# Kernel optimization log

Measured on AMD Instinct MI355X. Metric: run time of the kernel, lower is better.

Reference implementation:

```python
import jax, jax.numpy as jnp
import numpy as np

IP = 10  # power-iteration steps


def setup_inputs() -> dict:
    key = jax.random.key(0)
    k1, k2 = jax.random.split(key)
    B, C, H, W = 16, 512, 64, 64
    x = jax.random.normal(k1, (B, C, H, W), dtype=jnp.float32)
    # random start vector for power iteration (torch: FloatTensor.normal_(0,1))
    v = jax.random.normal(k2, (B, C, 1), dtype=jnp.float32)
    return {"x": x, "v": v}


def reference(x, v):
    B, C, H, W = x.shape
    # w = x.view(B,C,HW).permute(0,2,1) -> (B, HW, C)
    w = jnp.transpose(x.reshape(B, C, H * W), (0, 2, 1))
    # W_s = w^T w : (B, C, C)
    Ws = jnp.einsum('bnc,bnd->bcd', w, w)

    def step(vc, _):
        vc = jnp.matmul(Ws, vc)                                   # (B,C,1)
        vc = vc / jnp.linalg.norm(vc, axis=(1, 2), keepdims=True)  # per-batch L2 norm
        return vc, None

    v, _ = jax.lax.scan(step, v, None, length=IP)
    # u = W v, normalized : (B, HW, 1)
    u = jnp.matmul(w, v)
    u = u / jnp.linalg.norm(u, axis=(1, 2), keepdims=True)
    # z = u v^T : (B, HW, C) -> (B, C, H, W)
    z = jnp.matmul(u, jnp.transpose(v, (0, 2, 1)))
    z = jnp.transpose(z, (0, 2, 1)).reshape(B, C, H, W)
    return x + z
```

## Files before the change

kernel.cpp:

```cpp
#include <hip/hip_runtime.h>
#include <stdint.h>

#define NB 16
#define NC 512
#define NHW 4096

typedef unsigned short u16;
typedef __bf16 bf16x8 __attribute__((ext_vector_type(8)));
typedef float f32x4 __attribute__((ext_vector_type(4)));
typedef unsigned short u16x8 __attribute__((ext_vector_type(8)));
typedef unsigned short u16x4 __attribute__((ext_vector_type(4)));

#define AS1 __attribute__((address_space(1)))
#define AS3 __attribute__((address_space(3)))

__device__ __forceinline__ float bf2f(u16 h) {
    union { unsigned u; float f; } a; a.u = ((unsigned)h) << 16; return a.f;
}
__device__ __forceinline__ u16 f2bf(float f) {
    union { float f; unsigned u; } a; a.f = f;
    unsigned u = a.u;
    return (u16)((u + 0x7FFFu + ((u >> 16) & 1u)) >> 16);
}

__global__ __launch_bounds__(256) void k_to_bf16(const float* __restrict__ x,
                                                 u16* __restrict__ xb) {
    int i = blockIdx.x * 256 + threadIdx.x;
    f32x4 v = ((const f32x4*)x)[i];
    u16x4 o;
    o[0] = f2bf(v[0]); o[1] = f2bf(v[1]); o[2] = f2bf(v[2]); o[3] = f2bf(v[3]);
    ((u16x4*)xb)[i] = o;
}

__global__ __launch_bounds__(256, 1)
void k_gemm_bt(const u16* __restrict__ Ab, const u16* __restrict__ Bb,
               u16* __restrict__ Cb, int K, int N,
               size_t sA, size_t sB, size_t sC, float scale) {
    __shared__ u16 As[4][128 * 32];
    __shared__ u16 Bs[4][128 * 32];
    const int tid = threadIdx.x;
    const int wave = tid >> 6, lane = tid & 63;
    const int b = blockIdx.z;
    const u16* A  = Ab + (size_t)b * sA + (size_t)blockIdx.x * 128 * K;
    const u16* Bm = Bb + (size_t)b * sB + (size_t)blockIdx.y * 128 * K;

    const int srow = tid >> 2;
    const int scol = ((tid & 3) ^ ((srow >> 1) & 3)) * 8;
    const u16* ag0 = A  + (size_t)srow * K + scol;
    const u16* ag1 = ag0 + (size_t)64 * K;
    const u16* bg0 = Bm + (size_t)srow * K + scol;
    const u16* bg1 = bg0 + (size_t)64 * K;

#define STAGE(BUF, KO)                                                         \
    {                                                                          \
        __builtin_amdgcn_global_load_lds((AS1 void*)(ag0 + (KO)),              \
            (AS3 void*)(&As[BUF][wave * 512]), 16, 0, 0);                      \
        __builtin_amdgcn_global_load_lds((AS1 void*)(ag1 + (KO)),              \
            (AS3 void*)(&As[BUF][2048 + wave * 512]), 16, 0, 0);               \
        __builtin_amdgcn_global_load_lds((AS1 void*)(bg0 + (KO)),              \
            (AS3 void*)(&Bs[BUF][wave * 512]), 16, 0, 0);                      \
        __builtin_amdgcn_global_load_lds((AS1 void*)(bg1 + (KO)),              \
            (AS3 void*)(&Bs[BUF][2048 + wave * 512]), 16, 0, 0);               \
    }

    f32x4 acc[4][4];
#pragma unroll
    for (int i = 0; i < 4; i++)
#pragma unroll
        for (int j = 0; j < 4; j++) acc[i][j] = f32x4{0.f, 0.f, 0.f, 0.f};

    const int rm = (wave & 1) * 64;
    const int rn = (wave >> 1) * 64;
    const int m16 = lane & 15, quad = lane >> 4;
    const int qsw8 = (quad ^ ((m16 >> 1) & 3)) * 8;

#define COMPUTE(BUF)                                                           \
    {                                                                          \
        bf16x8 af[4], bfr[4];                                                  \
        _Pragma("unroll")                                                      \
        for (int mi = 0; mi < 4; mi++)                                         \
            af[mi] = *(const bf16x8*)&As[BUF][(rm + mi * 16 + m16) * 32 +      \
                                             qsw8];                            \
        _Pragma("unroll")                                                      \
        for (int ni = 0; ni < 4; ni++)                                         \
            bfr[ni] = *(const bf16x8*)&Bs[BUF][(rn + ni * 16 + m16) * 32 +     \
                                              qsw8];                           \
        _Pragma("unroll")                                                      \
        for (int mi = 0; mi < 4; mi++)                                         \
            _Pragma("unroll")                                                  \
            for (int ni = 0; ni < 4; ni++)                                     \
                acc[mi][ni] = __builtin_amdgcn_mfma_f32_16x16x32_bf16(         \
                    af[mi], bfr[ni], acc[mi][ni], 0, 0, 0);                    \
    }

#define PHASE(J, KNEXT)                                                        \
    asm volatile("s_waitcnt vmcnt(12)" ::: "memory");                          \
    __builtin_amdgcn_s_barrier();                                              \
    __builtin_amdgcn_sched_barrier(0);                                         \
    COMPUTE(J);                                                                \
    __builtin_amdgcn_sched_barrier(0);                                         \
    __builtin_amdgcn_s_barrier();                                              \
    STAGE(J, KNEXT);

    STAGE(0, 0);
    STAGE(1, 32);
    STAGE(2, 64);
    STAGE(3, 96);

    for (int kg = 0; kg + 256 <= K; kg += 128) {
        PHASE(0, kg + 128);
        PHASE(1, kg + 160);
        PHASE(2, kg + 192);
        PHASE(3, kg + 224);
    }

    asm volatile("s_waitcnt vmcnt(12)" ::: "memory");
    __builtin_amdgcn_s_barrier();
    __builtin_amdgcn_sched_barrier(0);
    COMPUTE(0);
    asm volatile("s_waitcnt vmcnt(8)" ::: "memory");
    __builtin_amdgcn_s_barrier();
    __builtin_amdgcn_sched_barrier(0);
    COMPUTE(1);
    asm volatile("s_waitcnt vmcnt(4)" ::: "memory");
    __builtin_amdgcn_s_barrier();
    __builtin_amdgcn_sched_barrier(0);
    COMPUTE(2);
    asm volatile("s_waitcnt vmcnt(0)" ::: "memory");
    __builtin_amdgcn_s_barrier();
    __builtin_amdgcn_sched_barrier(0);
    COMPUTE(3);

    u16* Co = Cb + (size_t)b * sC + ((size_t)blockIdx.x * 128) * N +
              (size_t)blockIdx.y * 128;
    const int rq = quad * 4;
#pragma unroll
    for (int mi = 0; mi < 4; mi++)
#pragma unroll
        for (int ni = 0; ni < 4; ni++)
#pragma unroll
            for (int r = 0; r < 4; r++) {
                int row = rm + mi * 16 + rq + r;
                int col = rn + ni * 16 + m16;
                Co[(size_t)row * N + col] = f2bf(acc[mi][ni][r] * scale);
            }
#undef STAGE
#undef COMPUTE
#undef PHASE
}

__global__ __launch_bounds__(1024, 1)
void k_power_iter(const u16* __restrict__ S2, const float* __restrict__ v0,
                  float* __restrict__ vhat) {
    const int b = blockIdx.x, tid = threadIdx.x;
    __shared__ float va[NC], vb[NC];
    __shared__ float part[NC][16];
    __shared__ float red[16];
    const u16* Mb = S2 + (size_t)b * NC * NC;
    const int cg = tid & 15;
    const int r0 = tid >> 4;
    if (tid < NC) va[tid] = v0[b * NC + tid];
    float* cur = va;
    float* nxt = vb;
    __syncthreads();

    for (int it = 0; it < 5; ++it) {
        float c[4][8];
#pragma unroll
        for (int p = 0; p < 4; p++) {
            f32x4 lo = *(const f32x4*)&cur[cg * 8 + p * 128];
            f32x4 hi = *(const f32x4*)&cur[cg * 8 + p * 128 + 4];
            c[p][0] = lo[0]; c[p][1] = lo[1]; c[p][2] = lo[2]; c[p][3] = lo[3];
            c[p][4] = hi[0]; c[p][5] = hi[1]; c[p][6] = hi[2]; c[p][7] = hi[3];
        }
#pragma unroll 2
        for (int pass = 0; pass < 8; ++pass) {
            const int r = pass * 64 + r0;
            const u16* row = Mb + (size_t)r * NC + cg * 8;
            u16x8 m[4];
#pragma unroll
            for (int p = 0; p < 4; p++) m[p] = *(const u16x8*)(row + p * 128);
            float a0 = 0.f, a1 = 0.f, a2 = 0.f, a3 = 0.f;
#pragma unroll
            for (int j = 0; j < 8; j++) {
                a0 += bf2f(m[0][j]) * c[0][j];
                a1 += bf2f(m[1][j]) * c[1][j];
                a2 += bf2f(m[2][j]) * c[2][j];
                a3 += bf2f(m[3][j]) * c[3][j];
            }
            part[r][cg] = (a0 + a1) + (a2 + a3);
        }
        __syncthreads();
        if (tid < NC) {
            f32x4 s0 = *(const f32x4*)&part[tid][0];
            f32x4 s1 = *(const f32x4*)&part[tid][4];
            f32x4 s2 = *(const f32x4*)&part[tid][8];
            f32x4 s3 = *(const f32x4*)&part[tid][12];
            f32x4 s = (s0 + s1) + (s2 + s3);
            nxt[tid] = (s[0] + s[1]) + (s[2] + s[3]);
        }
        __syncthreads();
        float* t = cur; cur = nxt; nxt = t;
    }

    float mv = (tid < NC) ? cur[tid] : 0.f;
    float x = mv * mv;
#pragma unroll
    for (int o = 32; o > 0; o >>= 1) x += __shfl_down(x, o, 64);
    if ((tid & 63) == 0) red[tid >> 6] = x;
    __syncthreads();
    float n = red[0];
#pragma unroll
    for (int w = 1; w < 16; w++) n += red[w];
    if (tid < NC) vhat[b * NC + tid] = mv * rsqrtf(n);
}

__global__ __launch_bounds__(256)
void k_compute_t(const u16* __restrict__ xb, const float* __restrict__ vhat,
                 float* __restrict__ tp) {
    const int b = blockIdx.z, cc = blockIdx.y, nc = blockIdx.x, tid = threadIdx.x;
    __shared__ float vsh[128];
    if (tid < 128) vsh[tid] = vhat[b * NC + cc * 128 + tid];
    __syncthreads();
    const int n0 = nc * 2048 + tid * 8;
    const u16* xp = xb + (size_t)b * NC * NHW + (size_t)cc * 128 * NHW + n0;
    float acc[8] = {0.f, 0.f, 0.f, 0.f, 0.f, 0.f, 0.f, 0.f};
    for (int c = 0; c < 128; c++) {
        u16x8 w = *(const u16x8*)xp;
        xp += NHW;
        float vc = vsh[c];
#pragma unroll
        for (int j = 0; j < 8; j++) acc[j] += bf2f(w[j]) * vc;
    }
    float* dst = tp + (size_t)(b * 4 + cc) * NHW + n0;
    *(f32x4*)dst       = f32x4{acc[0], acc[1], acc[2], acc[3]};
    *(f32x4*)(dst + 4) = f32x4{acc[4], acc[5], acc[6], acc[7]};
}

__global__ __launch_bounds__(1024, 1)
void k_tnorm(const float* __restrict__ tp, float* __restrict__ tsum,
             float* __restrict__ sinv) {
    const int b = blockIdx.x, tid = threadIdx.x;
    __shared__ float red[16];
    const int n0 = tid * 4;
    f32x4 s = f32x4{0.f, 0.f, 0.f, 0.f};
#pragma unroll
    for (int p = 0; p < 4; p++)
        s += *(const f32x4*)(tp + (size_t)(b * 4 + p) * NHW + n0);
    *(f32x4*)(tsum + (size_t)b * NHW + n0) = s;
    float ss = s[0] * s[0] + s[1] * s[1] + s[2] * s[2] + s[3] * s[3];
#pragma unroll
    for (int o = 32; o > 0; o >>= 1) ss += __shfl_down(ss, o, 64);
    if ((tid & 63) == 0) red[tid >> 6] = ss;
    __syncthreads();
    if (tid == 0) {
        float n = red[0];
#pragma unroll
        for (int w = 1; w < 16; w++) n += red[w];
        sinv[b] = rsqrtf(n);
    }
}

__global__ __launch_bounds__(256)
void k_epilogue(const float* __restrict__ x, const float* __restrict__ tsum,
                const float* __restrict__ vhat, const float* __restrict__ sinv,
                float* __restrict__ out) {
    const int b = blockIdx.z, cc = blockIdx.y, nc = blockIdx.x, tid = threadIdx.x;
    __shared__ float tl[1024];
    __shared__ float cf[64];
    const int nbase = nc * 1024, cbase = cc * 64;
    const float si = sinv[b];
    for (int i = tid; i < 1024; i += 256)
        tl[i] = tsum[(size_t)b * NHW + nbase + i];
    if (tid < 64) cf[tid] = vhat[b * NC + cbase + tid] * si;
    __syncthreads();
    f32x4 tv = ((const f32x4*)tl)[tid];
    for (int rr = 0; rr < 64; rr++) {
        size_t off = ((size_t)(b * NC + cbase + rr)) * NHW + nbase + tid * 4;
        f32x4 xv = *(const f32x4*)(x + off);
        float c = cf[rr];
        f32x4 o = xv + tv * c;
        *(f32x4*)(out + off) = o;
    }
}

extern "C" void kernel_launch(void* const* d_in, const int* in_sizes, int n_in,
                              void* d_out, int out_size, void* d_ws, size_t ws_size,
                              hipStream_t stream) {
    const float* x  = (const float*)d_in[0];
    const float* v0 = (const float*)d_in[1];
    float* out = (float*)d_out;

    char* ws = (char*)d_ws;
    u16* xb     = (u16*)ws;
    u16* S      = (u16*)(ws + 67108864);
    u16* S2     = (u16*)(ws + 67108864 + 8388608);
    float* vhat = (float*)(ws + 83886080);
    float* tp   = (float*)(ws + 83886080 + 65536);
    float* tsum = (float*)(ws + 83886080 + 65536 + 1048576);
    float* sinv = (float*)(ws + 83886080 + 65536 + 1048576 + 262144);

    k_to_bf16<<<dim3(32768), dim3(256), 0, stream>>>(x, xb);
    k_gemm_bt<<<dim3(4, 4, NB), dim3(256), 0, stream>>>(
        xb, xb, S, NHW, NC, (size_t)NC * NHW, (size_t)NC * NHW, (size_t)NC * NC,
        1.f / 4096.f);
    k_gemm_bt<<<dim3(4, 4, NB), dim3(256), 0, stream>>>(
        S, S, S2, NC, NC, (size_t)NC * NC, (size_t)NC * NC, (size_t)NC * NC,
        1.f);
    k_power_iter<<<dim3(NB), dim3(1024), 0, stream>>>(S2, v0, vhat);
    k_compute_t<<<dim3(2, 4, NB), dim3(256), 0, stream>>>(xb, vhat, tp);
    k_tnorm<<<dim3(NB), dim3(1024), 0, stream>>>(tp, tsum, sinv);
    k_epilogue<<<dim3(4, 8, NB), dim3(256), 0, stream>>>(x, tsum, vhat, sinv, out);
}
```

Before: 395.0 us.

## Split-K the Gram GEMM four ways with a separate reduction kernel

The x·xᵀ Gram GEMM, which launched only 256 blocks on a large GPU, is split along K into four slices. That gives 1024 blocks, each writing fp32 partials into the output buffer used as scratch. A new kernel sums the partials, scales them and converts to bf16. Both GEMMs now use a 2-stage LDS pipeline instead of 4 stages, with launch bounds allowing 4 blocks per CU for higher occupancy. The cost is an extra 64 MB of fp32 partial traffic and one extra launch.

```diff
diff --git a/kernel.cpp b/kernel.cpp
--- a/kernel.cpp
+++ b/kernel.cpp
@@ -32,59 +32,28 @@
     ((u16x4*)xb)[i] = o;
 }
 
-__global__ __launch_bounds__(256, 1)
-void k_gemm_bt(const u16* __restrict__ Ab, const u16* __restrict__ Bb,
-               u16* __restrict__ Cb, int K, int N,
-               size_t sA, size_t sB, size_t sC, float scale) {
-    __shared__ u16 As[4][128 * 32];
-    __shared__ u16 Bs[4][128 * 32];
-    const int tid = threadIdx.x;
-    const int wave = tid >> 6, lane = tid & 63;
-    const int b = blockIdx.z;
-    const u16* A  = Ab + (size_t)b * sA + (size_t)blockIdx.x * 128 * K;
-    const u16* Bm = Bb + (size_t)b * sB + (size_t)blockIdx.y * 128 * K;
-
-    const int srow = tid >> 2;
-    const int scol = ((tid & 3) ^ ((srow >> 1) & 3)) * 8;
-    const u16* ag0 = A  + (size_t)srow * K + scol;
-    const u16* ag1 = ag0 + (size_t)64 * K;
-    const u16* bg0 = Bm + (size_t)srow * K + scol;
-    const u16* bg1 = bg0 + (size_t)64 * K;
-
-#define STAGE(BUF, KO)                                                         \
+
+#define STAGE_BODY(ASb, BSb, KO)                                               \
     {                                                                          \
         __builtin_amdgcn_global_load_lds((AS1 void*)(ag0 + (KO)),              \
-            (AS3 void*)(&As[BUF][wave * 512]), 16, 0, 0);                      \
+            (AS3 void*)(&(ASb)[wave * 512]), 16, 0, 0);                        \
         __builtin_amdgcn_global_load_lds((AS1 void*)(ag1 + (KO)),              \
-            (AS3 void*)(&As[BUF][2048 + wave * 512]), 16, 0, 0);               \
+            (AS3 void*)(&(ASb)[2048 + wave * 512]), 16, 0, 0);                 \
         __builtin_amdgcn_global_load_lds((AS1 void*)(bg0 + (KO)),              \
-            (AS3 void*)(&Bs[BUF][wave * 512]), 16, 0, 0);                      \
+            (AS3 void*)(&(BSb)[wave * 512]), 16, 0, 0);                        \
         __builtin_amdgcn_global_load_lds((AS1 void*)(bg1 + (KO)),              \
-            (AS3 void*)(&Bs[BUF][2048 + wave * 512]), 16, 0, 0);               \
-    }
-
-    f32x4 acc[4][4];
-#pragma unroll
-    for (int i = 0; i < 4; i++)
-#pragma unroll
-        for (int j = 0; j < 4; j++) acc[i][j] = f32x4{0.f, 0.f, 0.f, 0.f};
-
-    const int rm = (wave & 1) * 64;
-    const int rn = (wave >> 1) * 64;
-    const int m16 = lane & 15, quad = lane >> 4;
-    const int qsw8 = (quad ^ ((m16 >> 1) & 3)) * 8;
-
-#define COMPUTE(BUF)                                                           \
+            (AS3 void*)(&(BSb)[2048 + wave * 512]), 16, 0, 0);                 \
+    }
+
+#define COMPUTE_BODY(ASb, BSb)                                                 \
     {                                                                          \
         bf16x8 af[4], bfr[4];                                                  \
         _Pragma("unroll")                                                      \
         for (int mi = 0; mi < 4; mi++)                                         \
-            af[mi] = *(const bf16x8*)&As[BUF][(rm + mi * 16 + m16) * 32 +      \
-                                             qsw8];                            \
+            af[mi] = *(const bf16x8*)&(ASb)[(rm + mi * 16 + m16) * 32 + qsw8]; \
         _Pragma("unroll")                                                      \
         for (int ni = 0; ni < 4; ni++)                                         \
-            bfr[ni] = *(const bf16x8*)&Bs[BUF][(rn + ni * 16 + m16) * 32 +     \
-                                              qsw8];                           \
+            bfr[ni] = *(const bf16x8*)&(BSb)[(rn + ni * 16 + m16) * 32 + qsw8];\
         _Pragma("unroll")                                                      \
         for (int mi = 0; mi < 4; mi++)                                         \
             _Pragma("unroll")                                                  \
@@ -93,46 +62,72 @@
                     af[mi], bfr[ni], acc[mi][ni], 0, 0, 0);                    \
     }
 
-#define PHASE(J, KNEXT)                                                        \
-    asm volatile("s_waitcnt vmcnt(12)" ::: "memory");                          \
+#define WAIT4_BAR()                                                            \
+    asm volatile("s_waitcnt vmcnt(4)" ::: "memory");                           \
     __builtin_amdgcn_s_barrier();                                              \
+    __builtin_amdgcn_sched_barrier(0);
+
+#define WAIT0_BAR()                                                            \
+    asm volatile("s_waitcnt vmcnt(0)" ::: "memory");                           \
+    __builtin_amdgcn_s_barrier();                                              \
+    __builtin_amdgcn_sched_barrier(0);
+
+#define END_BAR()                                                              \
     __builtin_amdgcn_sched_barrier(0);                                         \
-    COMPUTE(J);                                                                \
-    __builtin_amdgcn_sched_barrier(0);                                         \
-    __builtin_amdgcn_s_barrier();                                              \
-    STAGE(J, KNEXT);
-
-    STAGE(0, 0);
-    STAGE(1, 32);
-    STAGE(2, 64);
-    STAGE(3, 96);
-
-    for (int kg = 0; kg + 256 <= K; kg += 128) {
-        PHASE(0, kg + 128);
-        PHASE(1, kg + 160);
-        PHASE(2, kg + 192);
-        PHASE(3, kg + 224);
-    }
-
-    asm volatile("s_waitcnt vmcnt(12)" ::: "memory");
     __builtin_amdgcn_s_barrier();
-    __builtin_amdgcn_sched_barrier(0);
-    COMPUTE(0);
-    asm volatile("s_waitcnt vmcnt(8)" ::: "memory");
-    __builtin_amdgcn_s_barrier();
-    __builtin_amdgcn_sched_barrier(0);
-    COMPUTE(1);
-    asm volatile("s_waitcnt vmcnt(4)" ::: "memory");
-    __builtin_amdgcn_s_barrier();
-    __builtin_amdgcn_sched_barrier(0);
-    COMPUTE(2);
-    asm volatile("s_waitcnt vmcnt(0)" ::: "memory");
-    __builtin_amdgcn_s_barrier();
-    __builtin_amdgcn_sched_barrier(0);
-    COMPUTE(3);
-
-    u16* Co = Cb + (size_t)b * sC + ((size_t)blockIdx.x * 128) * N +
-              (size_t)blockIdx.y * 128;
+
+__global__ __launch_bounds__(256, 4)
+void k_gemm_xxt(const u16* __restrict__ Ab, float* __restrict__ P) {
+    __shared__ u16 As[2][128 * 32];
+    __shared__ u16 Bs[2][128 * 32];
+    const int tid = threadIdx.x;
+    const int wave = tid >> 6, lane = tid & 63;
+    const int b = blockIdx.z >> 2;
+    const int s = blockIdx.z & 3;
+    const int kBeg = s << 10;
+    const int kEnd = kBeg + 1024;
+
+    const u16* A  = Ab + (size_t)b * NC * NHW + (size_t)blockIdx.x * 128 * NHW;
+    const u16* Bm = Ab + (size_t)b * NC * NHW + (size_t)blockIdx.y * 128 * NHW;
+
+    const int srow = tid >> 2;
+    const int scol = ((tid & 3) ^ ((srow >> 1) & 3)) * 8;
+    const u16* ag0 = A  + (size_t)srow * NHW + scol;
+    const u16* ag1 = ag0 + (size_t)64 * NHW;
+    const u16* bg0 = Bm + (size_t)srow * NHW + scol;
+    const u16* bg1 = bg0 + (size_t)64 * NHW;
+
+    f32x4 acc[4][4];
+#pragma unroll
+    for (int i = 0; i < 4; i++)
+#pragma unroll
+        for (int j = 0; j < 4; j++) acc[i][j] = f32x4{0.f, 0.f, 0.f, 0.f};
+
+    const int rm = (wave & 1) * 64;
+    const int rn = (wave >> 1) * 64;
+    const int m16 = lane & 15, quad = lane >> 4;
+    const int qsw8 = (quad ^ ((m16 >> 1) & 3)) * 8;
+
+    STAGE_BODY(As[0], Bs[0], kBeg);
+    STAGE_BODY(As[1], Bs[1], kBeg + 32);
+
+    for (int kg = kBeg; kg + 128 <= kEnd; kg += 64) {
+        WAIT4_BAR();
+        COMPUTE_BODY(As[0], Bs[0]);
+        END_BAR();
+        STAGE_BODY(As[0], Bs[0], kg + 64);
+        WAIT4_BAR();
+        COMPUTE_BODY(As[1], Bs[1]);
+        END_BAR();
+        STAGE_BODY(As[1], Bs[1], kg + 96);
+    }
+    WAIT4_BAR();
+    COMPUTE_BODY(As[0], Bs[0]);
+    WAIT0_BAR();
+    COMPUTE_BODY(As[1], Bs[1]);
+
+    float* Po = P + ((size_t)s * NB + b) * NC * NC +
+                ((size_t)blockIdx.x * 128) * NC + (size_t)blockIdx.y * 128;
     const int rq = quad * 4;
 #pragma unroll
     for (int mi = 0; mi < 4; mi++)
@@ -142,11 +137,84 @@
             for (int r = 0; r < 4; r++) {
                 int row = rm + mi * 16 + rq + r;
                 int col = rn + ni * 16 + m16;
-                Co[(size_t)row * N + col] = f2bf(acc[mi][ni][r] * scale);
+                Po[(size_t)row * NC + col] = acc[mi][ni][r];
             }
-#undef STAGE
-#undef COMPUTE
-#undef PHASE
+}
+
+__global__ __launch_bounds__(256, 4)
+void k_gemm_ss(const u16* __restrict__ Sb, u16* __restrict__ S2) {
+    __shared__ u16 As[2][128 * 32];
+    __shared__ u16 Bs[2][128 * 32];
+    const int tid = threadIdx.x;
+    const int wave = tid >> 6, lane = tid & 63;
+    const int b = blockIdx.z;
+
+    const u16* A  = Sb + (size_t)b * NC * NC + (size_t)blockIdx.x * 128 * NC;
+    const u16* Bm = Sb + (size_t)b * NC * NC + (size_t)blockIdx.y * 128 * NC;
+
+    const int srow = tid >> 2;
+    const int scol = ((tid & 3) ^ ((srow >> 1) & 3)) * 8;
+    const u16* ag0 = A  + (size_t)srow * NC + scol;
+    const u16* ag1 = ag0 + (size_t)64 * NC;
+    const u16* bg0 = Bm + (size_t)srow * NC + scol;
+    const u16* bg1 = bg0 + (size_t)64 * NC;
+
+    f32x4 acc[4][4];
+#pragma unroll
+    for (int i = 0; i < 4; i++)
+#pragma unroll
+        for (int j = 0; j < 4; j++) acc[i][j] = f32x4{0.f, 0.f, 0.f, 0.f};
+
+    const int rm = (wave & 1) * 64;
+    const int rn = (wave >> 1) * 64;
+    const int m16 = lane & 15, quad = lane >> 4;
+    const int qsw8 = (quad ^ ((m16 >> 1) & 3)) * 8;
+
+    STAGE_BODY(As[0], Bs[0], 0);
+    STAGE_BODY(As[1], Bs[1], 32);
+
+    for (int kg = 0; kg + 128 <= NC; kg += 64) {
+        WAIT4_BAR();
+        COMPUTE_BODY(As[0], Bs[0]);
+        END_BAR();
+        STAGE_BODY(As[0], Bs[0], kg + 64);
+        WAIT4_BAR();
+        COMPUTE_BODY(As[1], Bs[1]);
+        END_BAR();
+        STAGE_BODY(As[1], Bs[1], kg + 96);
+    }
+    WAIT4_BAR();
+    COMPUTE_BODY(As[0], Bs[0]);
+    WAIT0_BAR();
+    COMPUTE_BODY(As[1], Bs[1]);
+
+    u16* Co = S2 + (size_t)b * NC * NC + ((size_t)blockIdx.x * 128) * NC +
+              (size_t)blockIdx.y * 128;
+    const int rq = quad * 4;
+#pragma unroll
+    for (int mi = 0; mi < 4; mi++)
+#pragma unroll
+        for (int ni = 0; ni < 4; ni++)
+#pragma unroll
+            for (int r = 0; r < 4; r++) {
+                int row = rm + mi * 16 + rq + r;
+                int col = rn + ni * 16 + m16;
+                Co[(size_t)row * NC + col] = f2bf(acc[mi][ni][r]);
+            }
+}
+
+__global__ __launch_bounds__(256)
+void k_reduce_S(const float* __restrict__ P, u16* __restrict__ S, float scale) {
+    const size_t g = (size_t)blockIdx.x * 256 + threadIdx.x;
+    const size_t stride = (size_t)NB * NC * NC / 4;
+    f32x4 t = ((const f32x4*)P)[g];
+    t += ((const f32x4*)P)[g + stride];
+    t += ((const f32x4*)P)[g + 2 * stride];
+    t += ((const f32x4*)P)[g + 3 * stride];
+    u16x4 o;
+    o[0] = f2bf(t[0] * scale); o[1] = f2bf(t[1] * scale);
+    o[2] = f2bf(t[2] * scale); o[3] = f2bf(t[3] * scale);
+    ((u16x4*)S)[g] = o;
 }
 
 __global__ __launch_bounds__(1024, 1)
@@ -300,13 +368,12 @@
     float* tsum = (float*)(ws + 83886080 + 65536 + 1048576);
     float* sinv = (float*)(ws + 83886080 + 65536 + 1048576 + 262144);
 
+    float* Pp = (float*)d_out;
+
     k_to_bf16<<<dim3(32768), dim3(256), 0, stream>>>(x, xb);
-    k_gemm_bt<<<dim3(4, 4, NB), dim3(256), 0, stream>>>(
-        xb, xb, S, NHW, NC, (size_t)NC * NHW, (size_t)NC * NHW, (size_t)NC * NC,
-        1.f / 4096.f);
-    k_gemm_bt<<<dim3(4, 4, NB), dim3(256), 0, stream>>>(
-        S, S, S2, NC, NC, (size_t)NC * NC, (size_t)NC * NC, (size_t)NC * NC,
-        1.f);
+    k_gemm_xxt<<<dim3(4, 4, NB * 4), dim3(256), 0, stream>>>(xb, Pp);
+    k_reduce_S<<<dim3(4096), dim3(256), 0, stream>>>(Pp, S, 1.f / 4096.f);
+    k_gemm_ss<<<dim3(4, 4, NB), dim3(256), 0, stream>>>(S, S2);
     k_power_iter<<<dim3(NB), dim3(1024), 0, stream>>>(S2, v0, vhat);
     k_compute_t<<<dim3(2, 4, NB), dim3(256), 0, stream>>>(xb, vhat, tp);
     k_tnorm<<<dim3(NB), dim3(1024), 0, stream>>>(tp, tsum, sinv);
```

Result: slower. 407.4 us (+3.1%).
